# Kernel tuning notes

Measured on AMD Instinct MI355X. Metric: run time of the kernel, lower is better.

## Reference

```python
import jax, jax.numpy as jnp
import numpy as np

LEAKY_SLOPE = 0.2
MASK_VAL = -9e15


def setup_inputs() -> dict:
    key = jax.random.key(0)
    k1, k2, k3, k4, k5, k6 = jax.random.split(key, 6)
    N_ex, N_kc, F_in, F_out = 20000, 1024, 128, 128
    exercise_h = jax.random.normal(k1, (N_ex, F_in), dtype=jnp.float32)
    kc_h = jax.random.normal(k2, (N_kc, F_in), dtype=jnp.float32)
    adj_exercise_kc = jax.random.randint(k3, (N_ex, N_kc), 0, 2, dtype=jnp.int32)
    # learned params (kaiming-ish scale)
    W1 = jax.random.normal(k4, (F_in, F_out), dtype=jnp.float32) * np.sqrt(2.0 / F_in)
    E = jax.random.normal(k5, (F_in, F_out), dtype=jnp.float32) * np.sqrt(2.0 / F_in)
    a = jax.random.normal(k6, (2 * F_out, 1), dtype=jnp.float32) * np.sqrt(2.0 / (2 * F_out))
    return {"exercise_h": exercise_h, "kc_h": kc_h,
            "adj_exercise_kc": adj_exercise_kc, "W1": W1, "E": E, "a": a}


def reference(exercise_h, kc_h, adj_exercise_kc, W1, E, a):
    F_out = W1.shape[1]
    kc_Wh = kc_h @ W1              # [N_kc, F_out]
    ex_Wh = exercise_h @ W1        # [N_ex, F_out]
    # Decompose a into halves: cat([ex_Wh_i, kc_Wh_j]) @ a == ex_Wh_i@a1 + kc_Wh_j@a2.
    a1, a2 = a[:F_out, 0], a[F_out:, 0]
    e = jax.nn.leaky_relu(ex_Wh @ a1[:, None] + (kc_Wh @ a2)[None, :],
                          negative_slope=LEAKY_SLOPE)   # [N_ex, N_kc]
    e = jnp.where(adj_exercise_kc > 0, e, MASK_VAL)
    attention = jax.nn.softmax(e, axis=1)
    new_kc_embed = attention @ kc_Wh               # [N_ex, F_out]
    exercise_Eh = exercise_h @ E                   # mode == 2
    return jax.nn.elu(new_kc_embed * exercise_Eh)
```

## Files before the change

kernel.cpp:

```cpp
#include <hip/hip_runtime.h>
#include <math.h>

#define N_EXC   20000
#define N_KCC   1024
#define FDIM    128
#define LEAKY_S 0.2f

#define BR  32
#define TJ  128
#define EXS 136

typedef unsigned short ushort_t;
typedef __attribute__((ext_vector_type(8))) short short8;
typedef __attribute__((ext_vector_type(4))) float floatx4;

__device__ __forceinline__ ushort_t f2bf(float f) {
    unsigned u = __float_as_uint(f);
    u += 0x7FFF + ((u >> 16) & 1);
    return (ushort_t)(u >> 16);
}

__device__ __forceinline__ void async16(const void* g, void* l) {
    __builtin_amdgcn_global_load_lds(
        (const __attribute__((address_space(1))) unsigned int*)g,
        (__attribute__((address_space(3))) unsigned int*)l,
        16, 0, 0);
}


__global__ __launch_bounds__(256) void gat_prep(const float* __restrict__ kc_h,
                                                const float* __restrict__ W1,
                                                const float* __restrict__ E,
                                                const float* __restrict__ a,
                                                float* __restrict__ ws)
{
    float* tarr = ws;
    float* w1a1 = ws + N_KCC;
    ushort_t* kc_sw = (ushort_t*)(ws + N_KCC + FDIM);
    ushort_t* E_sw  = kc_sw + FDIM * N_KCC;
    const int tid = threadIdx.x;
    const int b = blockIdx.x;

    __shared__ __align__(16) float kct[128 * 132];
    __shared__ __align__(16) ushort_t sw[32 * 128];
    __shared__ __align__(16) float w1a2_lds[FDIM];

    if (b < 32) {
        const int jb = b >> 2, fq = b & 3;
        const float* kcbase = kc_h + (size_t)jb * 128 * FDIM;
        #pragma unroll
        for (int u = 0; u < 16; ++u) {
            int flat = u * 256 + tid;
            int r = flat >> 5, c4 = (flat & 31) * 4;
            float4 v = *(const float4*)(kcbase + r * FDIM + c4);
            kct[r * 132 + c4 + 0] = v.x; kct[r * 132 + c4 + 1] = v.y;
            kct[r * 132 + c4 + 2] = v.z; kct[r * 132 + c4 + 3] = v.w;
        }
        __syncthreads();
        const int jg = tid >> 4;
        const int fg = tid & 15;
        const int f0 = fq * 32 + fg * 2;
        float acc[8][2];
        #pragma unroll
        for (int i = 0; i < 8; ++i) { acc[i][0] = 0.f; acc[i][1] = 0.f; }
        for (int k4 = 0; k4 < FDIM; k4 += 4) {
            float4 av[8];
            #pragma unroll
            for (int i = 0; i < 8; ++i)
                av[i] = *(const float4*)(kct + (jg * 8 + i) * 132 + k4);
            #pragma unroll
            for (int kk = 0; kk < 4; ++kk) {
                float2 bv = *(const float2*)(W1 + (k4 + kk) * FDIM + f0);
                #pragma unroll
                for (int i = 0; i < 8; ++i) {
                    float a_ = ((const float*)&av[i])[kk];
                    acc[i][0] += a_ * bv.x;
                    acc[i][1] += a_ * bv.y;
                }
            }
        }
        #pragma unroll
        for (int c = 0; c < 2; ++c) {
            int f = f0 + c;
            int fl = fg * 2 + c;
            unsigned pk[4];
            #pragma unroll
            for (int i = 0; i < 4; ++i)
                pk[i] = (unsigned)f2bf(acc[2 * i][c]) | ((unsigned)f2bf(acc[2 * i + 1][c]) << 16);
            int cp = jg ^ (f & 15);
            *(uint4*)(sw + fl * 128 + cp * 8) = make_uint4(pk[0], pk[1], pk[2], pk[3]);
        }
        __syncthreads();
        ushort_t* dst = kc_sw + ((size_t)jb * 128 + fq * 32) * 128;
        #pragma unroll
        for (int u = 0; u < 2; ++u) {
            int flat = u * 256 + tid;
            *(uint4*)(dst + flat * 8) = *(const uint4*)(sw + flat * 8);
        }
        return;
    }

    if (b < 36) {
        if (tid >= 128) {
            int k = tid - 128;
            float acc = 0.f;
            const float* row = W1 + k * FDIM;
            #pragma unroll 8
            for (int f = 0; f < FDIM; ++f) acc += row[f] * a[FDIM + f];
            w1a2_lds[k] = acc;
        } else if (b == 32) {
            float acc = 0.f;
            const float* row = W1 + tid * FDIM;
            #pragma unroll 8
            for (int f = 0; f < FDIM; ++f) acc += row[f] * a[f];
            w1a1[tid] = acc;
        }
        __syncthreads();
        int j = (b - 32) * 256 + tid;
        float s = 0.f;
        #pragma unroll 8
        for (int c = 0; c < 32; ++c) {
            float4 v = *(const float4*)(kc_h + (size_t)j * FDIM + c * 4);
            s += v.x * w1a2_lds[c * 4 + 0] + v.y * w1a2_lds[c * 4 + 1]
               + v.z * w1a2_lds[c * 4 + 2] + v.w * w1a2_lds[c * 4 + 3];
        }
        tarr[j] = s;
        return;
    }

    #pragma unroll
    for (int u = 0; u < 8; ++u) {
        int ch = u * 256 + tid;
        int n = ch >> 4, cp = ch & 15;
        int c = cp ^ (n & 15);
        unsigned pk[4];
        #pragma unroll
        for (int i = 0; i < 4; ++i) {
            float e0 = E[(c * 8 + 2 * i + 0) * FDIM + n];
            float e1 = E[(c * 8 + 2 * i + 1) * FDIM + n];
            pk[i] = (unsigned)f2bf(e0) | ((unsigned)f2bf(e1) << 16);
        }
        *(uint4*)(E_sw + ch * 8) = make_uint4(pk[0], pk[1], pk[2], pk[3]);
    }
}

__global__ __launch_bounds__(256, 3) void gat_main(const float* __restrict__ ex_h,
                                                   const int* __restrict__ adj,
                                                   const float* __restrict__ ws,
                                                   float* __restrict__ out)
{
    const float* tarr = ws;
    const float* w1a1 = ws + N_KCC;
    const ushort_t* kc_sw = (const ushort_t*)(ws + N_KCC + FDIM);
    const ushort_t* E_sw  = kc_sw + FDIM * N_KCC;

    __shared__ __align__(16) float t_lds[N_KCC];
    __shared__ __align__(16) ushort_t kc_lds[FDIM * TJ];
    __shared__ __align__(16) ushort_t exw_lds[BR * EXS];
    __shared__ __align__(16) float scrA[256];
    __shared__ __align__(16) float scrB[256];
    __shared__ float w1a1_lds[FDIM];
    __shared__ float s_lds[BR], m_lds[BR], denom_lds[BR];

    const int tid  = threadIdx.x;
    const int R0   = blockIdx.x * BR;
    const int lane = tid & 63, wid = tid >> 6;
    const int l15  = lane & 15, quad = lane >> 4;

    #pragma unroll
    for (int u = 0; u < 8; ++u) {
        int ci = u * 256 + tid;
        async16(E_sw + ci * 8, kc_lds + ci * 8);
    }

    #pragma unroll
    for (int u = 0; u < 4; ++u) t_lds[u * 256 + tid] = tarr[u * 256 + tid];
    if (tid < FDIM) w1a1_lds[tid] = w1a1[tid];
    const int r0 = tid >> 3;
    const int fc = (tid & 7) * 16;
    float exv[16];
    {
        const float* src = ex_h + (size_t)(R0 + r0) * FDIM + fc;
        #pragma unroll
        for (int c = 0; c < 4; ++c) {
            float4 v = *(const float4*)(src + c * 4);
            exv[c * 4 + 0] = v.x; exv[c * 4 + 1] = v.y;
            exv[c * 4 + 2] = v.z; exv[c * 4 + 3] = v.w;
        }
        unsigned pk[8];
        #pragma unroll
        for (int i = 0; i < 8; ++i)
            pk[i] = (unsigned)f2bf(exv[2 * i]) | ((unsigned)f2bf(exv[2 * i + 1]) << 16);
        *(uint4*)(exw_lds + r0 * EXS + fc)     = make_uint4(pk[0], pk[1], pk[2], pk[3]);
        *(uint4*)(exw_lds + r0 * EXS + fc + 8) = make_uint4(pk[4], pk[5], pk[6], pk[7]);
    }
    __syncthreads();

    {
        float mx = fmaxf(fmaxf(t_lds[tid], t_lds[256 + tid]),
                         fmaxf(t_lds[512 + tid], t_lds[768 + tid]));
        scrB[tid] = mx;
        float p = 0.f;
        #pragma unroll
        for (int i = 0; i < 16; ++i) p += exv[i] * w1a1_lds[fc + i];
        scrA[tid] = p;
    }
    __syncthreads();
    if (tid < 64)
        scrB[tid] = fmaxf(fmaxf(scrB[tid], scrB[tid + 64]),
                          fmaxf(scrB[tid + 128], scrB[tid + 192]));
    __syncthreads();
    if (tid < BR) {
        float Tm = scrB[0];
        #pragma unroll 8
        for (int i = 1; i < 64; ++i) Tm = fmaxf(Tm, scrB[i]);
        float s = 0.f;
        #pragma unroll
        for (int g = 0; g < 8; ++g) s += scrA[tid * 8 + g];
        s_lds[tid] = s;
        float x = s + Tm;
        m_lds[tid] = (x >= 0.f) ? x : LEAKY_S * x;
    }
    __syncthreads();

    floatx4 eh_acc[2][2], att_acc[2][2];
    #pragma unroll
    for (int mg = 0; mg < 2; ++mg)
        #pragma unroll
        for (int h = 0; h < 2; ++h) {
            eh_acc[mg][h]  = (floatx4){0.f, 0.f, 0.f, 0.f};
            att_acc[mg][h] = (floatx4){0.f, 0.f, 0.f, 0.f};
        }
    #pragma unroll
    for (int kk = 0; kk < 4; ++kk) {
        short8 a0 = *(const short8*)(exw_lds + l15 * EXS + kk * 32 + quad * 8);
        short8 a1 = *(const short8*)(exw_lds + (16 + l15) * EXS + kk * 32 + quad * 8);
        #pragma unroll
        for (int h = 0; h < 2; ++h) {
            const int n = (h * 4 + wid) * 16 + l15;
            const int cp = (kk * 4 + quad) ^ l15;
            short8 bf = *(const short8*)(kc_lds + n * TJ + cp * 8);
            eh_acc[0][h] = __builtin_amdgcn_mfma_f32_16x16x32_bf16(a0, bf, eh_acc[0][h], 0, 0, 0);
            eh_acc[1][h] = __builtin_amdgcn_mfma_f32_16x16x32_bf16(a1, bf, eh_acc[1][h], 0, 0, 0);
        }
    }

    const int r_w = tid >> 3;
    const int jg  = tid & 7;
    const float sr = s_lds[r_w];
    const float mr = m_lds[r_w];
    float denom_part = 0.f;
    const int* aptr = adj + (size_t)(R0 + r_w) * N_KCC + jg * 16;
    int4 cur0 = *(const int4*)(aptr + 0);
    int4 cur1 = *(const int4*)(aptr + 4);
    int4 cur2 = *(const int4*)(aptr + 8);
    int4 cur3 = *(const int4*)(aptr + 12);

    for (int jt = 0; jt < N_KCC / TJ; ++jt) {
        const int j0 = jt * TJ;
        __syncthreads();
        {
            const ushort_t* gsrc = kc_sw + (size_t)jt * (FDIM * TJ);
            #pragma unroll
            for (int u = 0; u < 8; ++u) {
                int ci = u * 256 + tid;
                async16(gsrc + ci * 8, kc_lds + ci * 8);
            }
        }
        {
            const int jb = j0 + jg * 16;
            int av[16] = {cur0.x, cur0.y, cur0.z, cur0.w, cur1.x, cur1.y, cur1.z, cur1.w,
                          cur2.x, cur2.y, cur2.z, cur2.w, cur3.x, cur3.y, cur3.z, cur3.w};
            float wv[16];
            #pragma unroll
            for (int c = 0; c < 4; ++c) {
                float4 t4 = *(const float4*)(t_lds + jb + c * 4);
                float tv[4] = {t4.x, t4.y, t4.z, t4.w};
                #pragma unroll
                for (int e = 0; e < 4; ++e) {
                    float x = sr + tv[e];
                    x = fmaxf(x, LEAKY_S * x);
                    float w = __expf(x - mr);
                    w = (av[c * 4 + e] > 0) ? w : 0.f;
                    denom_part += w;
                    wv[c * 4 + e] = w;
                }
            }
            unsigned pk[8];
            #pragma unroll
            for (int i = 0; i < 8; ++i) {
                unsigned ua = __float_as_uint(wv[2 * i + 0]) + 0x8000u;
                unsigned ub = __float_as_uint(wv[2 * i + 1]) + 0x8000u;
                pk[i] = __builtin_amdgcn_perm(ub, ua, 0x07060302);
            }
            *(uint4*)(exw_lds + r_w * EXS + jg * 16)     = make_uint4(pk[0], pk[1], pk[2], pk[3]);
            *(uint4*)(exw_lds + r_w * EXS + jg * 16 + 8) = make_uint4(pk[4], pk[5], pk[6], pk[7]);
        }
        __syncthreads();
        {
            int jn = (jt + 1 < N_KCC / TJ) ? (jt + 1) * TJ : jt * TJ;
            cur0 = *(const int4*)(aptr + jn + 0);
            cur1 = *(const int4*)(aptr + jn + 4);
            cur2 = *(const int4*)(aptr + jn + 8);
            cur3 = *(const int4*)(aptr + jn + 12);
        }
        #pragma unroll
        for (int kk = 0; kk < 4; ++kk) {
            short8 a0 = *(const short8*)(exw_lds + l15 * EXS + kk * 32 + quad * 8);
            short8 a1 = *(const short8*)(exw_lds + (16 + l15) * EXS + kk * 32 + quad * 8);
            #pragma unroll
            for (int h = 0; h < 2; ++h) {
                const int f = (h * 4 + wid) * 16 + l15;
                const int cp = (kk * 4 + quad) ^ l15;
                short8 bf = *(const short8*)(kc_lds + f * TJ + cp * 8);
                att_acc[0][h] = __builtin_amdgcn_mfma_f32_16x16x32_bf16(a0, bf, att_acc[0][h], 0, 0, 0);
                att_acc[1][h] = __builtin_amdgcn_mfma_f32_16x16x32_bf16(a1, bf, att_acc[1][h], 0, 0, 0);
            }
        }
    }

    __syncthreads();
    scrA[tid] = denom_part;
    __syncthreads();
    if (tid < BR) {
        float d = 0.f;
        #pragma unroll
        for (int g = 0; g < 8; ++g) d += scrA[tid * 8 + g];
        denom_lds[tid] = (d > 0.f) ? d : 1.f;
    }
    __syncthreads();

    #pragma unroll
    for (int mg = 0; mg < 2; ++mg) {
        float rd[4];
        #pragma unroll
        for (int reg = 0; reg < 4; ++reg)
            rd[reg] = 1.f / denom_lds[mg * 16 + quad * 4 + reg];
        #pragma unroll
        for (int h = 0; h < 2; ++h) {
            const int col = (h * 4 + wid) * 16 + l15;
            #pragma unroll
            for (int reg = 0; reg < 4; ++reg) {
                const int rl = mg * 16 + quad * 4 + reg;
                float v = att_acc[mg][h][reg] * rd[reg] * eh_acc[mg][h][reg];
                out[(size_t)(R0 + rl) * FDIM + col] = (v > 0.f) ? v : expm1f(v);
            }
        }
    }
}

extern "C" void kernel_launch(void* const* d_in, const int* in_sizes, int n_in,
                              void* d_out, int out_size, void* d_ws, size_t ws_size,
                              hipStream_t stream)
{
    const float* ex_h = (const float*)d_in[0];
    const float* kc_h = (const float*)d_in[1];
    const int*   adj  = (const int*)d_in[2];
    const float* W1   = (const float*)d_in[3];
    const float* E    = (const float*)d_in[4];
    const float* a    = (const float*)d_in[5];
    float* outp = (float*)d_out;
    float* ws   = (float*)d_ws;

    gat_prep<<<37, 256, 0, stream>>>(kc_h, W1, E, a, ws);
    gat_main<<<N_EXC / BR, 256, 0, stream>>>(ex_h, adj, ws, outp);
}
```

Baseline: 158.0 us.

## Double-buffer kc tiles with TJ=64 and precompute adjacency bitmasks up front

Halves the j-tile to 64 and double-buffers both the kc_Wh tile and the attention-weight tile in LDS, so the async load and weight generation for tile jt+1 overlap the MFMAs on tile jt. The loop now needs one barrier per iteration instead of two. The whole adjacency row slice is loaded once at kernel start and packed into 32-bit masks, removing the per-iteration int loads from the loop. The precompute swizzle is changed to 64-wide tiles to match. This raises LDS use and register pressure, doubles the number of loop iterations, and puts all adjacency loads before any compute.

```diff
diff --git a/kernel.cpp b/kernel.cpp
--- a/kernel.cpp
+++ b/kernel.cpp
@@ -7,8 +7,9 @@
 #define LEAKY_S 0.2f
 
 #define BR  32
-#define TJ  128
+#define TJ  64
 #define EXS 136
+#define WST 72
 
 typedef unsigned short ushort_t;
 typedef __attribute__((ext_vector_type(8))) short short8;
@@ -87,15 +88,20 @@
             #pragma unroll
             for (int i = 0; i < 4; ++i)
                 pk[i] = (unsigned)f2bf(acc[2 * i][c]) | ((unsigned)f2bf(acc[2 * i + 1][c]) << 16);
-            int cp = jg ^ (f & 15);
-            *(uint4*)(sw + fl * 128 + cp * 8) = make_uint4(pk[0], pk[1], pk[2], pk[3]);
+            int jtl = jg >> 3;
+            int cpp = (jg & 7) ^ (f & 7);
+            *(uint4*)(sw + fl * 128 + jtl * 64 + cpp * 8) = make_uint4(pk[0], pk[1], pk[2], pk[3]);
         }
         __syncthreads();
-        ushort_t* dst = kc_sw + ((size_t)jb * 128 + fq * 32) * 128;
         #pragma unroll
         for (int u = 0; u < 2; ++u) {
             int flat = u * 256 + tid;
-            *(uint4*)(dst + flat * 8) = *(const uint4*)(sw + flat * 8);
+            int fl = flat >> 4;
+            int rem = flat & 15;
+            int jtl = rem >> 3, cpp = rem & 7;
+            ushort_t* dst = kc_sw + ((size_t)(jb * 2 + jtl)) * 8192
+                          + (fq * 32 + fl) * 64 + cpp * 8;
+            *(uint4*)dst = *(const uint4*)(sw + flat * 8);
         }
         return;
     }
@@ -131,13 +137,16 @@
     #pragma unroll
     for (int u = 0; u < 8; ++u) {
         int ch = u * 256 + tid;
-        int n = ch >> 4, cp = ch & 15;
-        int c = cp ^ (n & 15);
+        int half = ch >> 10;
+        int rem = ch & 1023;
+        int n = rem >> 3, cpp = rem & 7;
+        int c = cpp ^ (n & 7);
+        int kbase = half * 64 + c * 8;
         unsigned pk[4];
         #pragma unroll
         for (int i = 0; i < 4; ++i) {
-            float e0 = E[(c * 8 + 2 * i + 0) * FDIM + n];
-            float e1 = E[(c * 8 + 2 * i + 1) * FDIM + n];
+            float e0 = E[(kbase + 2 * i + 0) * FDIM + n];
+            float e1 = E[(kbase + 2 * i + 1) * FDIM + n];
             pk[i] = (unsigned)f2bf(e0) | ((unsigned)f2bf(e1) << 16);
         }
         *(uint4*)(E_sw + ch * 8) = make_uint4(pk[0], pk[1], pk[2], pk[3]);
@@ -155,8 +164,8 @@
     const ushort_t* E_sw  = kc_sw + FDIM * N_KCC;
 
     __shared__ __align__(16) float t_lds[N_KCC];
-    __shared__ __align__(16) ushort_t kc_lds[FDIM * TJ];
-    __shared__ __align__(16) ushort_t exw_lds[BR * EXS];
+    __shared__ __align__(16) ushort_t kc_lds[2 * 8192];
+    __shared__ __align__(16) ushort_t ww_lds[4608];
     __shared__ __align__(16) float scrA[256];
     __shared__ __align__(16) float scrB[256];
     __shared__ float w1a1_lds[FDIM];
@@ -191,8 +200,42 @@
         #pragma unroll
         for (int i = 0; i < 8; ++i)
             pk[i] = (unsigned)f2bf(exv[2 * i]) | ((unsigned)f2bf(exv[2 * i + 1]) << 16);
-        *(uint4*)(exw_lds + r0 * EXS + fc)     = make_uint4(pk[0], pk[1], pk[2], pk[3]);
-        *(uint4*)(exw_lds + r0 * EXS + fc + 8) = make_uint4(pk[4], pk[5], pk[6], pk[7]);
+        *(uint4*)(ww_lds + r0 * EXS + fc)     = make_uint4(pk[0], pk[1], pk[2], pk[3]);
+        *(uint4*)(ww_lds + r0 * EXS + fc + 8) = make_uint4(pk[4], pk[5], pk[6], pk[7]);
+    }
+
+    const int r_w = tid >> 3;
+    const int jg  = tid & 7;
+    const int* abase = adj + (size_t)(R0 + r_w) * N_KCC + jg * 8;
+    unsigned msk[4];
+    #pragma unroll
+    for (int g = 0; g < 4; ++g) {
+        int4 q0 = *(const int4*)(abase + (g * 4 + 0) * 64);
+        int4 q1 = *(const int4*)(abase + (g * 4 + 0) * 64 + 4);
+        int4 q2 = *(const int4*)(abase + (g * 4 + 1) * 64);
+        int4 q3 = *(const int4*)(abase + (g * 4 + 1) * 64 + 4);
+        int4 q4 = *(const int4*)(abase + (g * 4 + 2) * 64);
+        int4 q5 = *(const int4*)(abase + (g * 4 + 2) * 64 + 4);
+        int4 q6 = *(const int4*)(abase + (g * 4 + 3) * 64);
+        int4 q7 = *(const int4*)(abase + (g * 4 + 3) * 64 + 4);
+        unsigned m = 0;
+        m |= (q0.x > 0 ? 1u : 0u) << 0;  m |= (q0.y > 0 ? 1u : 0u) << 1;
+        m |= (q0.z > 0 ? 1u : 0u) << 2;  m |= (q0.w > 0 ? 1u : 0u) << 3;
+        m |= (q1.x > 0 ? 1u : 0u) << 4;  m |= (q1.y > 0 ? 1u : 0u) << 5;
+        m |= (q1.z > 0 ? 1u : 0u) << 6;  m |= (q1.w > 0 ? 1u : 0u) << 7;
+        m |= (q2.x > 0 ? 1u : 0u) << 8;  m |= (q2.y > 0 ? 1u : 0u) << 9;
+        m |= (q2.z > 0 ? 1u : 0u) << 10; m |= (q2.w > 0 ? 1u : 0u) << 11;
+        m |= (q3.x > 0 ? 1u : 0u) << 12; m |= (q3.y > 0 ? 1u : 0u) << 13;
+        m |= (q3.z > 0 ? 1u : 0u) << 14; m |= (q3.w > 0 ? 1u : 0u) << 15;
+        m |= (q4.x > 0 ? 1u : 0u) << 16; m |= (q4.y > 0 ? 1u : 0u) << 17;
+        m |= (q4.z > 0 ? 1u : 0u) << 18; m |= (q4.w > 0 ? 1u : 0u) << 19;
+        m |= (q5.x > 0 ? 1u : 0u) << 20; m |= (q5.y > 0 ? 1u : 0u) << 21;
+        m |= (q5.z > 0 ? 1u : 0u) << 22; m |= (q5.w > 0 ? 1u : 0u) << 23;
+        m |= (q6.x > 0 ? 1u : 0u) << 24; m |= (q6.y > 0 ? 1u : 0u) << 25;
+        m |= (q6.z > 0 ? 1u : 0u) << 26; m |= (q6.w > 0 ? 1u : 0u) << 27;
+        m |= (q7.x > 0 ? 1u : 0u) << 28; m |= (q7.y > 0 ? 1u : 0u) << 29;
+        m |= (q7.z > 0 ? 1u : 0u) << 30; m |= (q7.w > 0 ? 1u : 0u) << 31;
+        msk[g] = m;
     }
     __syncthreads();
 
@@ -233,93 +276,86 @@
         }
     #pragma unroll
     for (int kk = 0; kk < 4; ++kk) {
-        short8 a0 = *(const short8*)(exw_lds + l15 * EXS + kk * 32 + quad * 8);
-        short8 a1 = *(const short8*)(exw_lds + (16 + l15) * EXS + kk * 32 + quad * 8);
+        short8 a0 = *(const short8*)(ww_lds + l15 * EXS + kk * 32 + quad * 8);
+        short8 a1 = *(const short8*)(ww_lds + (16 + l15) * EXS + kk * 32 + quad * 8);
         #pragma unroll
         for (int h = 0; h < 2; ++h) {
             const int n = (h * 4 + wid) * 16 + l15;
-            const int cp = (kk * 4 + quad) ^ l15;
-            short8 bf = *(const short8*)(kc_lds + n * TJ + cp * 8);
+            const int cpp = ((kk & 1) * 4 + quad) ^ (n & 7);
+            short8 bf = *(const short8*)(kc_lds + (kk >> 1) * 8192 + n * 64 + cpp * 8);
             eh_acc[0][h] = __builtin_amdgcn_mfma_f32_16x16x32_bf16(a0, bf, eh_acc[0][h], 0, 0, 0);
             eh_acc[1][h] = __builtin_amdgcn_mfma_f32_16x16x32_bf16(a1, bf, eh_acc[1][h], 0, 0, 0);
         }
     }
-
-    const int r_w = tid >> 3;
-    const int jg  = tid & 7;
+    __syncthreads();
+
     const float sr = s_lds[r_w];
     const float mr = m_lds[r_w];
     float denom_part = 0.f;
-    const int* aptr = adj + (size_t)(R0 + r_w) * N_KCC + jg * 16;
-    int4 cur0 = *(const int4*)(aptr + 0);
-    int4 cur1 = *(const int4*)(aptr + 4);
-    int4 cur2 = *(const int4*)(aptr + 8);
-    int4 cur3 = *(const int4*)(aptr + 12);
+
+    auto genw = [&](int jt, ushort_t* wb) {
+        const int jb = jt * TJ + jg * 8;
+        float4 ta = *(const float4*)(t_lds + jb);
+        float4 tb = *(const float4*)(t_lds + jb + 4);
+        float tv[8] = {ta.x, ta.y, ta.z, ta.w, tb.x, tb.y, tb.z, tb.w};
+        unsigned mb = msk[jt >> 2] >> ((jt & 3) * 8);
+        float wv[8];
+        #pragma unroll
+        for (int e = 0; e < 8; ++e) {
+            float x = sr + tv[e];
+            x = fmaxf(x, LEAKY_S * x);
+            float w = __expf(x - mr);
+            w = ((mb >> e) & 1u) ? w : 0.f;
+            denom_part += w;
+            wv[e] = w;
+        }
+        unsigned pk[4];
+        #pragma unroll
+        for (int i = 0; i < 4; ++i) {
+            unsigned ua = __float_as_uint(wv[2 * i + 0]) + 0x8000u;
+            unsigned ub = __float_as_uint(wv[2 * i + 1]) + 0x8000u;
+            pk[i] = __builtin_amdgcn_perm(ub, ua, 0x07060302);
+        }
+        *(uint4*)(wb + r_w * WST + jg * 8) = make_uint4(pk[0], pk[1], pk[2], pk[3]);
+    };
+
+    #pragma unroll
+    for (int u = 0; u < 4; ++u) {
+        int ci = u * 256 + tid;
+        async16(kc_sw + ci * 8, kc_lds + ci * 8);
+    }
+    genw(0, ww_lds);
+    __syncthreads();
 
     for (int jt = 0; jt < N_KCC / TJ; ++jt) {
-        const int j0 = jt * TJ;
-        __syncthreads();
-        {
-            const ushort_t* gsrc = kc_sw + (size_t)jt * (FDIM * TJ);
-            #pragma unroll
-            for (int u = 0; u < 8; ++u) {
+        if (jt < 15) {
+            const ushort_t* gsrc = kc_sw + (size_t)(jt + 1) * 8192;
+            ushort_t* kdst = kc_lds + ((jt + 1) & 1) * 8192;
+            #pragma unroll
+            for (int u = 0; u < 4; ++u) {
                 int ci = u * 256 + tid;
-                async16(gsrc + ci * 8, kc_lds + ci * 8);
+                async16(gsrc + ci * 8, kdst + ci * 8);
             }
-        }
-        {
-            const int jb = j0 + jg * 16;
-            int av[16] = {cur0.x, cur0.y, cur0.z, cur0.w, cur1.x, cur1.y, cur1.z, cur1.w,
-                          cur2.x, cur2.y, cur2.z, cur2.w, cur3.x, cur3.y, cur3.z, cur3.w};
-            float wv[16];
-            #pragma unroll
-            for (int c = 0; c < 4; ++c) {
-                float4 t4 = *(const float4*)(t_lds + jb + c * 4);
-                float tv[4] = {t4.x, t4.y, t4.z, t4.w};
-                #pragma unroll
-                for (int e = 0; e < 4; ++e) {
-                    float x = sr + tv[e];
-                    x = fmaxf(x, LEAKY_S * x);
-                    float w = __expf(x - mr);
-                    w = (av[c * 4 + e] > 0) ? w : 0.f;
-                    denom_part += w;
-                    wv[c * 4 + e] = w;
-                }
-            }
-            unsigned pk[8];
-            #pragma unroll
-            for (int i = 0; i < 8; ++i) {
-                unsigned ua = __float_as_uint(wv[2 * i + 0]) + 0x8000u;
-                unsigned ub = __float_as_uint(wv[2 * i + 1]) + 0x8000u;
-                pk[i] = __builtin_amdgcn_perm(ub, ua, 0x07060302);
-            }
-            *(uint4*)(exw_lds + r_w * EXS + jg * 16)     = make_uint4(pk[0], pk[1], pk[2], pk[3]);
-            *(uint4*)(exw_lds + r_w * EXS + jg * 16 + 8) = make_uint4(pk[4], pk[5], pk[6], pk[7]);
-        }
-        __syncthreads();
-        {
-            int jn = (jt + 1 < N_KCC / TJ) ? (jt + 1) * TJ : jt * TJ;
-            cur0 = *(const int4*)(aptr + jn + 0);
-            cur1 = *(const int4*)(aptr + jn + 4);
-            cur2 = *(const int4*)(aptr + jn + 8);
-            cur3 = *(const int4*)(aptr + jn + 12);
-        }
-        #pragma unroll
-        for (int kk = 0; kk < 4; ++kk) {
-            short8 a0 = *(const short8*)(exw_lds + l15 * EXS + kk * 32 + quad * 8);
-            short8 a1 = *(const short8*)(exw_lds + (16 + l15) * EXS + kk * 32 + quad * 8);
+            genw(jt + 1, ww_lds + ((jt + 1) & 1) * 2304);
+        }
+        const ushort_t* kcb = kc_lds + (jt & 1) * 8192;
+        const ushort_t* wb  = ww_lds + (jt & 1) * 2304;
+        #pragma unroll
+        for (int kk = 0; kk < 2; ++kk) {
+            short8 a0 = *(const short8*)(wb + l15 * WST + kk * 32 + quad * 8);
+            short8 a1 = *(const short8*)(wb + (16 + l15) * WST + kk * 32 + quad * 8);
             #pragma unroll
             for (int h = 0; h < 2; ++h) {
                 const int f = (h * 4 + wid) * 16 + l15;
-                const int cp = (kk * 4 + quad) ^ l15;
-                short8 bf = *(const short8*)(kc_lds + f * TJ + cp * 8);
+                const int cpp = (kk * 4 + quad) ^ (f & 7);
+                short8 bf = *(const short8*)(kcb + f * 64 + cpp * 8);
                 att_acc[0][h] = __builtin_amdgcn_mfma_f32_16x16x32_bf16(a0, bf, att_acc[0][h], 0, 0, 0);
                 att_acc[1][h] = __builtin_amdgcn_mfma_f32_16x16x32_bf16(a1, bf, att_acc[1][h], 0, 0, 0);
             }
         }
-    }
-
-    __syncthreads();
+        __syncthreads();
+    }
+
     scrA[tid] = denom_part;
     __syncthreads();
     if (tid < BR) {
```

Result: slower. 164.7 us (+4.3%).
